# Kernel optimization log

Hardware: AMD Instinct MI355X
Metric: run time of the kernel (lower is better)

Reference implementation:

```python
import jax, jax.numpy as jnp
import numpy as np

EPS = 1.1920929e-07  # torch fp32 finfo eps used by F.rms_norm default

def rms_norm(x):
    return x * jax.lax.rsqrt(jnp.mean(jnp.square(x), axis=-1, keepdims=True) + EPS)

def setup_inputs() -> dict:
    key = jax.random.key(0)
    kx, kfc, kpr, krt = jax.random.split(key, 4)
    B, T, C, F = 4, 2048, 2048, 8192
    s = (3.0 ** 0.5) * C ** -0.5  # init scale used in init_weights
    x = jax.random.normal(kx, (B, T, C), dtype=jnp.float32)
    w_fc = jax.random.normal(kfc, (F, C), dtype=jnp.float32) * s
    w_proj = jax.random.normal(kpr, (C, F), dtype=jnp.float32) * (s * 0.1)
    w_router = jax.random.normal(krt, (1, C), dtype=jnp.float32) * 0.01  # router init std=0.01
    return {"x": x, "w_fc": w_fc, "w_proj": w_proj, "w_router": w_router}

def reference(x, w_fc, w_proj, w_router):
    # Router: (B,T,C) @ (C,1) -> (B,T) logits; STE mask (~0 or ~1 floats)
    logits = jnp.einsum('btc,oc->bto', x, w_router)[..., 0]  # (B,T)
    prob = jax.nn.sigmoid(logits)
    hard = (prob > 0.5).astype(x.dtype)
    mask_i = hard + prob - jax.lax.stop_gradient(prob)  # straight-through
    mask_bool = mask_i > 0.5  # (B,T)

    # Gated MLP (mixture-of-depth). The torch code gathers selected tokens,
    # runs the MLP on the compacted set, scatters into zeros, and multiplies
    # by mask_i. Mathematically identical dense form (honoring the mask):
    h = jnp.einsum('btc,fc->btf', rms_norm(x), w_fc)
    h = jnp.square(jax.nn.relu(h))  # relu(x)^2 activation
    mlp_out = jnp.einsum('btf,cf->btc', h, w_proj)
    gated = jnp.where(mask_bool[..., None], mlp_out * mask_i[..., None], 0.0)
    return x + gated
```

## Files before the change

kernel.cpp:

```cpp
#include <hip/hip_runtime.h>
#include <type_traits>
#include <utility>
#include <stdint.h>
#include <stddef.h>

#define TOKENS 8192
#define CDIM 2048
#define FDIM 8192
#define EPSV 1.1920929e-07f

typedef __attribute__((ext_vector_type(8))) short short8;
typedef __attribute__((ext_vector_type(8))) __bf16 bf16x8;
typedef __attribute__((ext_vector_type(4))) float floatx4;
typedef __attribute__((ext_vector_type(4))) float f32x4;
typedef __attribute__((ext_vector_type(2))) unsigned int u32x2;

template <typename V, typename = void> struct CanMfma : std::false_type {};
template <typename V>
struct CanMfma<V, std::void_t<decltype(__builtin_amdgcn_mfma_f32_16x16x32_bf16(
    std::declval<V>(), std::declval<V>(), std::declval<floatx4>(), 0, 0, 0))>>
    : std::true_type {};
using frag_t = std::conditional_t<CanMfma<short8>::value, short8, bf16x8>;

__device__ __forceinline__ floatx4 mfma_bf16(frag_t a, frag_t b, floatx4 c) {
    return __builtin_amdgcn_mfma_f32_16x16x32_bf16(a, b, c, 0, 0, 0);
}

__device__ __forceinline__ unsigned short f2bf(float f) {
    unsigned int u = __float_as_uint(f);
    u += 0x7fffu + ((u >> 16) & 1u);
    return (unsigned short)(u >> 16);
}

__global__ void zero_kernel(int* p) { if (threadIdx.x == 0) *p = 0; }


__global__ __launch_bounds__(256) void cvt2_kernel(
    const float* __restrict__ s1, unsigned short* __restrict__ d1,
    const float* __restrict__ s2, unsigned short* __restrict__ d2)
{
    const int NC1 = FDIM * (CDIM / 8);
    int i = blockIdx.x * 256 + threadIdx.x;
    const float* src; unsigned short* dst;
    int n, t, PK, K8;
    if (i < NC1) { src = s1; dst = d1; n = i >> 8; t = i & 255; PK = 32; K8 = 256; }
    else { i -= NC1; src = s2; dst = d2; n = i >> 10; t = i & 1023; PK = 128; K8 = 1024; }
    const int kt = t >> 3, q8 = t & 7;
    const int r = n & 127, ni = n >> 7;
    const float4* sp = (const float4*)src + ((size_t)n * K8 + t) * 2;
    float4 v0 = sp[0], v1 = sp[1];
    short8 o;
    o[0] = (short)f2bf(v0.x); o[1] = (short)f2bf(v0.y);
    o[2] = (short)f2bf(v0.z); o[3] = (short)f2bf(v0.w);
    o[4] = (short)f2bf(v1.x); o[5] = (short)f2bf(v1.y);
    o[6] = (short)f2bf(v1.z); o[7] = (short)f2bf(v1.w);
    size_t di = (((size_t)ni * PK + kt) * 128 + r) * 64 + (size_t)((q8 ^ (r & 7)) << 3);
    __builtin_nontemporal_store(o, (short8*)(dst + di));
}

__global__ __launch_bounds__(256) void router_kernel(
    const float* __restrict__ x, const float* __restrict__ wr,
    float* __restrict__ out, unsigned short* __restrict__ Xn,
    int* __restrict__ idx, float* __restrict__ mv, int* __restrict__ cnt)
{
    const int token = blockIdx.x;
    const int tid = threadIdx.x;
    const float4* xr = (const float4*)(x + (size_t)token * CDIM);
    const float4* w4 = (const float4*)wr;
    float4 a0 = xr[2 * tid];
    float4 a1 = xr[2 * tid + 1];
    float4 b0 = w4[2 * tid];
    float4 b1 = w4[2 * tid + 1];
    float ss = a0.x*a0.x + a0.y*a0.y + a0.z*a0.z + a0.w*a0.w
             + a1.x*a1.x + a1.y*a1.y + a1.z*a1.z + a1.w*a1.w;
    float dt = a0.x*b0.x + a0.y*b0.y + a0.z*b0.z + a0.w*b0.w
             + a1.x*b1.x + a1.y*b1.y + a1.z*b1.z + a1.w*b1.w;
    #pragma unroll
    for (int off = 32; off > 0; off >>= 1) {
        ss += __shfl_down(ss, off);
        dt += __shfl_down(dt, off);
    }
    __shared__ float red_ss[4], red_dt[4];
    __shared__ float s_rms;
    __shared__ int s_pos;
    const int wave = tid >> 6;
    if ((tid & 63) == 0) { red_ss[wave] = ss; red_dt[wave] = dt; }
    __syncthreads();
    if (tid == 0) {
        float S = red_ss[0] + red_ss[1] + red_ss[2] + red_ss[3];
        float D = red_dt[0] + red_dt[1] + red_dt[2] + red_dt[3];
        float prob = 1.0f / (1.0f + expf(-D));
        s_rms = 1.0f / sqrtf(S * (1.0f / (float)CDIM) + EPSV);
        int pos = -1;
        if (prob > 0.5f) {
            pos = atomicAdd(cnt, 1);
            idx[pos] = token;
            mv[pos] = (1.0f + prob) - prob;
        }
        s_pos = pos;
    }
    __syncthreads();
    const float rms = s_rms;
    const int pos = s_pos;
    float* op = out + (size_t)token * CDIM;
    if (pos < 0) {
        f32x4 r0 = {a0.x, a0.y, a0.z, a0.w};
        f32x4 r1 = {a1.x, a1.y, a1.z, a1.w};
        __builtin_nontemporal_store(r0, (f32x4*)(op + tid * 8));
        __builtin_nontemporal_store(r1, (f32x4*)(op + tid * 8 + 4));
    } else {
        const int kt = tid >> 3, q8 = tid & 7;
        const int r = pos & 127, mi = pos >> 7;
        short8 o;
        o[0] = (short)f2bf(a0.x * rms); o[1] = (short)f2bf(a0.y * rms);
        o[2] = (short)f2bf(a0.z * rms); o[3] = (short)f2bf(a0.w * rms);
        o[4] = (short)f2bf(a1.x * rms); o[5] = (short)f2bf(a1.y * rms);
        o[6] = (short)f2bf(a1.z * rms); o[7] = (short)f2bf(a1.w * rms);
        size_t di = (((size_t)mi * 32 + kt) * 128 + r) * 64 + (size_t)((q8 ^ (r & 7)) << 3);
        __builtin_nontemporal_store(o, (short8*)(Xn + di));
    }
}

template <int K, int MODE, int LDO, int NP>
__global__ __launch_bounds__(512, 4) void gemm_bt(
    const unsigned short* __restrict__ A,
    const unsigned short* __restrict__ B,
    unsigned short* __restrict__ Hout,
    float* __restrict__ out,
    const float* __restrict__ xin,
    const int* __restrict__ idx,
    const float* __restrict__ mv,
    const int* __restrict__ cntp)
{
    const int cnt = *cntp;
    const int mp = (cnt + 127) >> 7;
    const int xcd = blockIdx.x & 7;
    const int wix = blockIdx.x >> 3;
    constexpr int NPX = NP / 8;
    const int tiles_slice = mp * NPX;
    const int crew = (int)gridDim.x >> 3;

    const int tid = threadIdx.x;
    const int wave = tid >> 6;
    const int lane = tid & 63;
    const int wm = (wave >> 2) * 64;
    const int wn = (wave & 3) * 32;
    const int quad = lane >> 4;
    const int l16 = lane & 15;

    __shared__ alignas(16) unsigned short lA[128 * 64];
    __shared__ alignas(16) unsigned short lB[128 * 64];

    constexpr int PK = K / 64;
    constexpr int NT = K / 64;

    for (int t = wix; t < tiles_slice; t += crew) {
        const int mi = t % mp;
        const int ni = xcd * NPX + t / mp;
        const int m0 = mi * 128;
        const int n0 = ni * 128;

        const unsigned short* aq = A + (size_t)mi * PK * 8192 + (size_t)tid * 8;
        const unsigned short* bq = B + (size_t)ni * PK * 8192 + (size_t)tid * 8;

        floatx4 acc[4][2] = {};

        for (int kt = 0; kt < NT; ++kt) {
            __builtin_amdgcn_global_load_lds(
                (__attribute__((address_space(1))) void*)aq,
                (__attribute__((address_space(3))) void*)&lA[(size_t)tid * 8],
                16, 0, 0);
            __builtin_amdgcn_global_load_lds(
                (__attribute__((address_space(1))) void*)(aq + 512 * 8),
                (__attribute__((address_space(3))) void*)&lA[((size_t)tid + 512) * 8],
                16, 0, 0);
            __builtin_amdgcn_global_load_lds(
                (__attribute__((address_space(1))) void*)bq,
                (__attribute__((address_space(3))) void*)&lB[(size_t)tid * 8],
                16, 0, 0);
            __builtin_amdgcn_global_load_lds(
                (__attribute__((address_space(1))) void*)(bq + 512 * 8),
                (__attribute__((address_space(3))) void*)&lB[((size_t)tid + 512) * 8],
                16, 0, 0);
            aq += 8192;
            bq += 8192;
            __syncthreads();
            #pragma unroll
            for (int st = 0; st < 2; ++st) {
                frag_t af[4], bfv[2];
                #pragma unroll
                for (int tt = 0; tt < 4; ++tt) {
                    const int ra = wm + tt * 16 + l16;
                    const int ca = ((st * 4 + quad) ^ (ra & 7)) * 8;
                    af[tt] = *(const frag_t*)&lA[ra * 64 + ca];
                }
                #pragma unroll
                for (int tt = 0; tt < 2; ++tt) {
                    const int rb = wn + tt * 16 + l16;
                    const int cb = ((st * 4 + quad) ^ (rb & 7)) * 8;
                    bfv[tt] = *(const frag_t*)&lB[rb * 64 + cb];
                }
                #pragma unroll
                for (int tm = 0; tm < 4; ++tm)
                    #pragma unroll
                    for (int tn = 0; tn < 2; ++tn)
                        acc[tm][tn] = mfma_bf16(af[tm], bfv[tn], acc[tm][tn]);
            }
            __syncthreads();
        }

        if (MODE == 1) {
            constexpr int PKH = LDO / 64;
            #pragma unroll
            for (int tm = 0; tm < 4; ++tm) {
                const int rbase = wm + tm * 16 + quad * 4;
                #pragma unroll
                for (int tn = 0; tn < 2; ++tn) {
                    const int gn = n0 + wn + tn * 16 + l16;
                    const int kt = gn >> 6, q8 = (gn >> 3) & 7, e = gn & 7;
                    #pragma unroll
                    for (int v = 0; v < 4; ++v) {
                        const int r = rbase + v;
                        float h = fmaxf(acc[tm][tn][v], 0.0f);
                        size_t di = (((size_t)mi * PKH + kt) * 128 + r) * 64
                                  + (size_t)((q8 ^ (r & 7)) << 3) + e;
                        __builtin_nontemporal_store(f2bf(h * h), &Hout[di]);
                    }
                }
            }
        } else {
            #pragma unroll
            for (int tm = 0; tm < 4; ++tm) {
                const int gmb = m0 + wm + tm * 16 + quad * 4;
                #pragma unroll
                for (int v = 0; v < 4; ++v) {
                    const int gm = gmb + v;
                    if (gm < cnt) {
                        const int token = idx[gm];
                        const float scale = mv[gm];
                        const float* xrow = xin + (size_t)token * LDO;
                        float* orow = out + (size_t)token * LDO;
                        #pragma unroll
                        for (int tn = 0; tn < 2; ++tn) {
                            const int gn = n0 + wn + tn * 16 + l16;
                            float r = xrow[gn] + scale * acc[tm][tn][v];
                            __builtin_nontemporal_store(r, &orow[gn]);
                        }
                    }
                }
            }
        }
    }
}

extern "C" void kernel_launch(void* const* d_in, const int* in_sizes, int n_in,
                              void* d_out, int out_size, void* d_ws, size_t ws_size,
                              hipStream_t stream)
{
    const float* x   = (const float*)d_in[0];
    const float* wfc = (const float*)d_in[1];
    const float* wpr = (const float*)d_in[2];
    const float* wrt = (const float*)d_in[3];
    float* out = (float*)d_out;

    char* ws = (char*)d_ws;
    int*   cnt = (int*)ws;
    int*   idx = (int*)(ws + 256);
    float* mv  = (float*)(ws + 256 + 32768);
    unsigned short* Xn  = (unsigned short*)(ws + 65792);
    unsigned short* Wfc = (unsigned short*)(ws + 65792 + 33554432ULL);
    unsigned short* Wpr = (unsigned short*)(ws + 65792 + 67108864ULL);
    unsigned short* H   = (unsigned short*)(ws + 65792 + 100663296ULL);

    const int nchunks = FDIM * (CDIM / 8) + CDIM * (FDIM / 8);
    zero_kernel<<<1, 64, 0, stream>>>(cnt);
    cvt2_kernel<<<nchunks / 256, 256, 0, stream>>>(wfc, Wfc, wpr, Wpr);
    router_kernel<<<TOKENS, 256, 0, stream>>>(x, wrt, out, Xn, idx, mv, cnt);
    gemm_bt<CDIM, 1, FDIM, FDIM / 128><<<512, 512, 0, stream>>>(
        Xn, Wfc, H, nullptr, nullptr, nullptr, nullptr, cnt);
    gemm_bt<FDIM, 2, CDIM, CDIM / 128><<<512, 512, 0, stream>>>(
        H, Wpr, nullptr, out, x, idx, mv, cnt);
}
```

Measured before the change: 748.3 us.

## Double-buffer GEMM LDS tiles with register prefetch instead of direct global-to-LDS loads

Result: faster. 698.1 us (-6.7%).

```diff
diff --git a/kernel.cpp b/kernel.cpp
--- a/kernel.cpp
+++ b/kernel.cpp
@@ -148,11 +148,15 @@
     const int quad = lane >> 4;
     const int l16 = lane & 15;
 
-    __shared__ alignas(16) unsigned short lA[128 * 64];
-    __shared__ alignas(16) unsigned short lB[128 * 64];
+    __shared__ alignas(16) unsigned short lA[2][128 * 64];
+    __shared__ alignas(16) unsigned short lB[2][128 * 64];
 
     constexpr int PK = K / 64;
     constexpr int NT = K / 64;
+    static_assert(NT % 2 == 0, "NT must be even");
+
+    const size_t c0 = (size_t)tid * 8;
+    const size_t c1 = (size_t)(tid + 512) * 8;
 
     for (int t = wix; t < tiles_slice; t += crew) {
         const int mi = t % mp;
@@ -160,31 +164,25 @@
         const int m0 = mi * 128;
         const int n0 = ni * 128;
 
-        const unsigned short* aq = A + (size_t)mi * PK * 8192 + (size_t)tid * 8;
-        const unsigned short* bq = B + (size_t)ni * PK * 8192 + (size_t)tid * 8;
+        const unsigned short* aq = A + (size_t)mi * PK * 8192;
+        const unsigned short* bq = B + (size_t)ni * PK * 8192;
+
+        short8 a0_0, a1_0, b0_0, b1_0;
+        short8 a0_1, a1_1, b0_1, b1_1;
+
+        a0_0 = *(const short8*)(aq + c0);  a1_0 = *(const short8*)(aq + c1);
+        b0_0 = *(const short8*)(bq + c0);  b1_0 = *(const short8*)(bq + c1);
+        a0_1 = *(const short8*)(aq + 8192 + c0);  a1_1 = *(const short8*)(aq + 8192 + c1);
+        b0_1 = *(const short8*)(bq + 8192 + c0);  b1_1 = *(const short8*)(bq + 8192 + c1);
+        *(short8*)&lA[0][c0] = a0_0;  *(short8*)&lA[0][c1] = a1_0;
+        *(short8*)&lB[0][c0] = b0_0;  *(short8*)&lB[0][c1] = b1_0;
+        asm volatile("s_waitcnt lgkmcnt(0)" ::: "memory");
+        __builtin_amdgcn_s_barrier();
+        asm volatile("" ::: "memory");
 
         floatx4 acc[4][2] = {};
 
-        for (int kt = 0; kt < NT; ++kt) {
-            __builtin_amdgcn_global_load_lds(
-                (__attribute__((address_space(1))) void*)aq,
-                (__attribute__((address_space(3))) void*)&lA[(size_t)tid * 8],
-                16, 0, 0);
-            __builtin_amdgcn_global_load_lds(
-                (__attribute__((address_space(1))) void*)(aq + 512 * 8),
-                (__attribute__((address_space(3))) void*)&lA[((size_t)tid + 512) * 8],
-                16, 0, 0);
-            __builtin_amdgcn_global_load_lds(
-                (__attribute__((address_space(1))) void*)bq,
-                (__attribute__((address_space(3))) void*)&lB[(size_t)tid * 8],
-                16, 0, 0);
-            __builtin_amdgcn_global_load_lds(
-                (__attribute__((address_space(1))) void*)(bq + 512 * 8),
-                (__attribute__((address_space(3))) void*)&lB[((size_t)tid + 512) * 8],
-                16, 0, 0);
-            aq += 8192;
-            bq += 8192;
-            __syncthreads();
+        auto compute = [&](int buf) {
             #pragma unroll
             for (int st = 0; st < 2; ++st) {
                 frag_t af[4], bfv[2];
@@ -192,13 +190,13 @@
                 for (int tt = 0; tt < 4; ++tt) {
                     const int ra = wm + tt * 16 + l16;
                     const int ca = ((st * 4 + quad) ^ (ra & 7)) * 8;
-                    af[tt] = *(const frag_t*)&lA[ra * 64 + ca];
+                    af[tt] = *(const frag_t*)&lA[buf][ra * 64 + ca];
                 }
                 #pragma unroll
                 for (int tt = 0; tt < 2; ++tt) {
                     const int rb = wn + tt * 16 + l16;
                     const int cb = ((st * 4 + quad) ^ (rb & 7)) * 8;
-                    bfv[tt] = *(const frag_t*)&lB[rb * 64 + cb];
+                    bfv[tt] = *(const frag_t*)&lB[buf][rb * 64 + cb];
                 }
                 #pragma unroll
                 for (int tm = 0; tm < 4; ++tm)
@@ -206,7 +204,36 @@
                     for (int tn = 0; tn < 2; ++tn)
                         acc[tm][tn] = mfma_bf16(af[tm], bfv[tn], acc[tm][tn]);
             }
-            __syncthreads();
+        };
+
+        for (int kt = 0; kt < NT; kt += 2) {
+            if (kt + 2 < NT) {
+                const unsigned short* a = aq + (size_t)(kt + 2) * 8192;
+                const unsigned short* b = bq + (size_t)(kt + 2) * 8192;
+                a0_0 = *(const short8*)(a + c0);  a1_0 = *(const short8*)(a + c1);
+                b0_0 = *(const short8*)(b + c0);  b1_0 = *(const short8*)(b + c1);
+            }
+            *(short8*)&lA[1][c0] = a0_1;  *(short8*)&lA[1][c1] = a1_1;
+            *(short8*)&lB[1][c0] = b0_1;  *(short8*)&lB[1][c1] = b1_1;
+            compute(0);
+            asm volatile("s_waitcnt lgkmcnt(0)" ::: "memory");
+            __builtin_amdgcn_s_barrier();
+            asm volatile("" ::: "memory");
+
+            if (kt + 3 < NT) {
+                const unsigned short* a = aq + (size_t)(kt + 3) * 8192;
+                const unsigned short* b = bq + (size_t)(kt + 3) * 8192;
+                a0_1 = *(const short8*)(a + c0);  a1_1 = *(const short8*)(a + c1);
+                b0_1 = *(const short8*)(b + c0);  b1_1 = *(const short8*)(b + c1);
+            }
+            if (kt + 2 < NT) {
+                *(short8*)&lA[0][c0] = a0_0;  *(short8*)&lA[0][c1] = a1_0;
+                *(short8*)&lB[0][c0] = b0_0;  *(short8*)&lB[0][c1] = b1_0;
+            }
+            compute(1);
+            asm volatile("s_waitcnt lgkmcnt(0)" ::: "memory");
+            __builtin_amdgcn_s_barrier();
+            asm volatile("" ::: "memory");
         }
 
         if (MODE == 1) {
```
